# Kernel optimization log

Measured on AMD Instinct MI355X. Metric: run time of the kernel, lower is better.

## Reference

```python
import jax, jax.numpy as jnp
import numpy as np

B, HOR, L, A, HID = 4096, 32, 512, 64, 1024


def _linear_params(key, fan_in, fan_out):
    kw, kb = jax.random.split(key)
    bound = 1.0 / np.sqrt(fan_in)
    W = jax.random.uniform(kw, (fan_in, fan_out), jnp.float32, -bound, bound)
    b = jax.random.uniform(kb, (fan_out,), jnp.float32, -bound, bound)
    return W, b


def setup_inputs() -> dict:
    key = jax.random.key(0)
    ks = jax.random.split(key, 11)
    initial_state = jax.random.normal(ks[0], (B, L), jnp.float32)
    action_sequence = jax.random.normal(ks[1], (B, HOR, A), jnp.float32)
    Wae, bae = _linear_params(ks[2], A, A)
    Wt1, bt1 = _linear_params(ks[3], L + A, HID)
    Wt2, bt2 = _linear_params(ks[4], HID, HID)
    Wt3, bt3 = _linear_params(ks[5], HID, L)
    Wo1, bo1 = _linear_params(ks[6], L, HID)
    Wo2, bo2 = _linear_params(ks[7], HID, L)
    Wh1, bh1 = _linear_params(ks[8], L + A, HID)
    Wh2, bh2 = _linear_params(ks[9], HID, 1)
    return dict(initial_state=initial_state, action_sequence=action_sequence,
                Wae=Wae, bae=bae, Wt1=Wt1, bt1=bt1, Wt2=Wt2, bt2=bt2,
                Wt3=Wt3, bt3=bt3, Wo1=Wo1, bo1=bo1, Wo2=Wo2, bo2=bo2,
                Wh1=Wh1, bh1=bh1, Wh2=Wh2, bh2=bh2)


def reference(initial_state, action_sequence, Wae, bae, Wt1, bt1, Wt2, bt2,
              Wt3, bt3, Wo1, bo1, Wo2, bo2, Wh1, bh1, Wh2, bh2):
    # rollout: sequential scan over horizon steps
    def step(state, action):
        # harm predictor on raw (state, action)
        sa = jnp.concatenate([state, action], axis=-1)            # [B, L+A]
        harm = jax.nn.sigmoid(jax.nn.relu(sa @ Wh1 + bh1) @ Wh2 + bh2)  # [B,1]
        # observation predictor on current state
        obs = jax.nn.relu(state @ Wo1 + bo1) @ Wo2 + bo2          # [B, L]
        # transition on (state, encoded action); residual update
        ae = action @ Wae + bae                                   # [B, A]
        sae = jnp.concatenate([state, ae], axis=-1)               # [B, L+A]
        h = jax.nn.relu(sae @ Wt1 + bt1)
        h = jax.nn.relu(h @ Wt2 + bt2)
        next_state = state + h @ Wt3 + bt3                        # [B, L]
        return next_state, (next_state, obs, harm[:, 0])

    actions_t = jnp.swapaxes(action_sequence, 0, 1)               # [HOR, B, A]
    _, (states_t, obs_t, harm_t) = jax.lax.scan(step, initial_state, actions_t)
    # states: initial + all next states -> [B, HOR+1, L]
    states = jnp.concatenate([initial_state[:, None, :],
                              jnp.swapaxes(states_t, 0, 1)], axis=1)
    observations = jnp.swapaxes(obs_t, 0, 1)                      # [B, HOR, L]
    harm_predictions = jnp.swapaxes(harm_t, 0, 1)                 # [B, HOR]
    return states, observations, harm_predictions
```

## Files before the change

kernel.cpp:

```cpp
#include <hip/hip_runtime.h>
#include <math.h>

#define B_ 4096
#define HOR_ 32
#define L_ 512
#define A_ 64
#define HID_ 1024

#define CB 512
#define MC (CB * HOR_)

typedef unsigned short ushort_t;
typedef __attribute__((ext_vector_type(4))) float f32x4;
typedef __attribute__((ext_vector_type(8))) short s16x8;
typedef __attribute__((ext_vector_type(4))) short s16x4;
typedef __attribute__((ext_vector_type(8))) _Float16 f16x8;

__device__ __forceinline__ unsigned short bf16_rne(float x) {
    unsigned u = __builtin_bit_cast(unsigned, x);
    u += 0x7fffu + ((u >> 16) & 1u);
    return (unsigned short)(u >> 16);
}
__device__ __forceinline__ float bf16_to_f32(unsigned short h) {
    unsigned u = ((unsigned)h) << 16;
    return __builtin_bit_cast(float, u);
}

__device__ __forceinline__ int xcd_swz(int bid, int nwg) {
    return (bid & 7) * (nwg >> 3) + (bid >> 3);
}

__device__ __forceinline__ void gld16(const void* g, void* l) {
    __builtin_amdgcn_global_load_lds(
        (const __attribute__((address_space(1))) void*)g,
        (__attribute__((address_space(3))) void*)l, 16, 0, 0);
}

template <int BMT, bool TWOSRC, bool SPLIT_OUT, bool RELU, bool RESID, bool F32OUT>
__global__ __launch_bounds__(512, 4) void trans_gemm(
    const _Float16* __restrict__ Ahi, const _Float16* __restrict__ Alo,
    int lda, int K,
    const float* __restrict__ Aae, int lda_ae, int aoff,
    const _Float16* __restrict__ Whi, const _Float16* __restrict__ Wlo,
    const float* __restrict__ bias,
    const float* __restrict__ resid, int ldr,
    _Float16* __restrict__ Ohi, _Float16* __restrict__ Olo, int ldoh,
    float* __restrict__ Of, int ldof)
{
    __shared__ _Float16 Ah[2][BMT][32];
    __shared__ _Float16 Al[2][BMT][32];
    __shared__ _Float16 Bh[2][64][32];
    __shared__ _Float16 Bl[2][64][32];

    const int gx = gridDim.x;
    const int bid = xcd_swz(blockIdx.y * gx + blockIdx.x, gx * gridDim.y);
    const int m0 = (bid / gx) * BMT;
    const int n0 = (bid % gx) * 64;

    const int tid = threadIdx.x;
    const int w = tid >> 6, l = tid & 63;
    const int wr = w >> 1, wc = w & 1;
    const int kg = l >> 4, lr = l & 15;
    constexpr int AF = BMT / 64;

    const bool doA = (BMT == 128) || (tid < 256);
    const bool doB = (BMT == 128) ? (tid < 256) : (tid >= 256);
    const int srowA = tid >> 2;
    const int srowB = (BMT == 128) ? (tid >> 2) : ((tid - 256) >> 2);
    const int sg = tid & 3;

    f32x4 acc[AF][2] = {};
    float4 e0, e1;

    const _Float16* pAh = Ahi + (size_t)(m0 + srowA) * lda + sg * 8;
    const _Float16* pAl = Alo + (size_t)(m0 + srowA) * lda + sg * 8;
    const _Float16* pBh = Whi + (size_t)(n0 + srowB) * K + sg * 8;
    const _Float16* pBl = Wlo + (size_t)(n0 + srowB) * K + sg * 8;
    const float* pAe = TWOSRC
        ? (Aae + (size_t)(m0 + srowA) * lda_ae + aoff + sg * 8 - L_)
        : nullptr;

    auto stage = [&](int buf, int ks) {
        const int k0 = ks * 32;
        if (doB) {
            gld16(pBh + k0, &Bh[buf][srowB][sg * 8]);
            gld16(pBl + k0, &Bl[buf][srowB][sg * 8]);
        }
        if (doA && (!TWOSRC || k0 < L_)) {
            gld16(pAh + k0, &Ah[buf][srowA][sg * 8]);
            gld16(pAl + k0, &Al[buf][srowA][sg * 8]);
        }
    };

    const int NT = K / 32;
    stage(0, 0);
    __syncthreads();
    int cur = 0;

    for (int ks = 0; ks < NT; ++ks) {
        const bool havepf = (ks + 1 < NT);
        const int k0n = (ks + 1) * 32;
        const bool aeNext = TWOSRC && havepf && (k0n >= L_);

        if (havepf) {
            stage(cur ^ 1, ks + 1);
            if (aeNext && doA) {
                e0 = *reinterpret_cast<const float4*>(pAe + k0n);
                e1 = *reinterpret_cast<const float4*>(pAe + k0n + 4);
            }
        }

        f16x8 ah[AF], al[AF], bh[2], bl[2];
#pragma unroll
        for (int i = 0; i < AF; ++i) {
            int r = wr * (BMT / 4) + i * 16 + lr;
            ah[i] = *reinterpret_cast<const f16x8*>(&Ah[cur][r][kg * 8]);
            al[i] = *reinterpret_cast<const f16x8*>(&Al[cur][r][kg * 8]);
        }
#pragma unroll
        for (int j = 0; j < 2; ++j) {
            int r = wc * 32 + j * 16 + lr;
            bh[j] = *reinterpret_cast<const f16x8*>(&Bh[cur][r][kg * 8]);
            bl[j] = *reinterpret_cast<const f16x8*>(&Bl[cur][r][kg * 8]);
        }
#pragma unroll
        for (int i = 0; i < AF; ++i)
#pragma unroll
            for (int j = 0; j < 2; ++j) {
                acc[i][j] = __builtin_amdgcn_mfma_f32_16x16x32_f16(
                    ah[i], bh[j], acc[i][j], 0, 0, 0);
                acc[i][j] = __builtin_amdgcn_mfma_f32_16x16x32_f16(
                    ah[i], bl[j], acc[i][j], 0, 0, 0);
                acc[i][j] = __builtin_amdgcn_mfma_f32_16x16x32_f16(
                    al[i], bh[j], acc[i][j], 0, 0, 0);
            }

        if (havepf) {
            if (aeNext && doA) {
                float vv[8] = {e0.x, e0.y, e0.z, e0.w, e1.x, e1.y, e1.z, e1.w};
                f16x8 h, lo;
#pragma unroll
                for (int j = 0; j < 8; ++j) {
                    _Float16 hh = (_Float16)vv[j];
                    h[j] = hh;
                    lo[j] = (_Float16)(vv[j] - (float)hh);
                }
                *reinterpret_cast<f16x8*>(&Ah[cur ^ 1][srowA][sg * 8]) = h;
                *reinterpret_cast<f16x8*>(&Al[cur ^ 1][srowA][sg * 8]) = lo;
            }
            __syncthreads();
            cur ^= 1;
        }
    }

    float bv[2];
#pragma unroll
    for (int j = 0; j < 2; ++j) bv[j] = bias[n0 + wc * 32 + j * 16 + lr];

#pragma unroll
    for (int i = 0; i < AF; ++i)
#pragma unroll
        for (int j = 0; j < 2; ++j)
#pragma unroll
            for (int r = 0; r < 4; ++r) {
                int row = m0 + wr * (BMT / 4) + i * 16 + kg * 4 + r;
                int col = n0 + wc * 32 + j * 16 + lr;
                float v = acc[i][j][r] + bv[j];
                if (RESID)
                    v += resid[(size_t)row * ldr + col];
                if (RELU) v = fmaxf(v, 0.f);
                if (F32OUT)
                    Of[(size_t)row * ldof + col] = v;
                if (SPLIT_OUT) {
                    _Float16 h = (_Float16)v;
                    Ohi[(size_t)row * ldoh + col] = h;
                    Olo[(size_t)row * ldoh + col] = (_Float16)(v - (float)h);
                }
            }
}

__global__ __launch_bounds__(256) void split_transpose(
    const float* __restrict__ W, _Float16* __restrict__ Whi,
    _Float16* __restrict__ Wlo, int K, int N)
{
    int k = blockIdx.x * 256 + threadIdx.x;
    int n = blockIdx.y;
    if (k < K) {
        float v = W[(size_t)k * N + n];
        _Float16 h = (_Float16)v;
        Whi[(size_t)n * K + k] = h;
        Wlo[(size_t)n * K + k] = (_Float16)(v - (float)h);
    }
}

__global__ __launch_bounds__(256) void ae_all(
    const float* __restrict__ actions,
    const float* __restrict__ Wae,
    const float* __restrict__ bae,
    float* __restrict__ ae)
{
    const long r = (long)blockIdx.x * 4 + (threadIdx.x >> 6);
    const int c = threadIdx.x & 63;
    const float* arow = actions + r * 64;
    float acc = bae[c];
#pragma unroll 16
    for (int k = 0; k < 64; ++k) acc = fmaf(arow[k], Wae[k * 64 + c], acc);
    ae[r * 64 + c] = acc;
}

__global__ __launch_bounds__(256) void ae_step(
    const float* __restrict__ actions, const float* __restrict__ Wae,
    const float* __restrict__ bae, int t, float* __restrict__ aeS)
{
    const long b = (long)blockIdx.x * 4 + (threadIdx.x >> 6);
    const int c = threadIdx.x & 63;
    const float* arow = actions + (b * HOR_ + t) * 64;
    float acc = bae[c];
#pragma unroll 16
    for (int k = 0; k < 64; ++k) acc = fmaf(arow[k], Wae[k * 64 + c], acc);
    aeS[b * 64 + c] = acc;
}

__global__ __launch_bounds__(256) void init_split(
    const float* __restrict__ init, float* __restrict__ states,
    _Float16* __restrict__ sth, _Float16* __restrict__ stl)
{
    size_t i = (size_t)blockIdx.x * 256 + threadIdx.x;
    size_t b = i >> 9, l = i & 511;
    float v = init[i];
    states[b * (33 * L_) + l] = v;
    _Float16 h = (_Float16)v;
    sth[i] = h;
    stl[i] = (_Float16)(v - (float)h);
}


__global__ __launch_bounds__(256) void cast_transpose(
    const float* __restrict__ W, ushort_t* __restrict__ WT, int K, int N)
{
    int k = blockIdx.x * 256 + threadIdx.x;
    int n = blockIdx.y;
    if (k < K) WT[(long)n * K + k] = bf16_rne(W[(long)k * N + n]);
}

__global__ __launch_bounds__(256) void mm_split(
    const float* __restrict__ Astate,
    const float* __restrict__ Aact,
    int Ktot,
    const ushort_t* __restrict__ WT,
    int N,
    const float* __restrict__ bias,
    ushort_t* __restrict__ Out)
{
    __shared__ ushort_t Ahi[128][40];
    __shared__ ushort_t Alo[128][40];
    __shared__ ushort_t Bt[128][40];

    const int tid = threadIdx.x;
    const int gx = gridDim.x;
    const int bid = xcd_swz(blockIdx.y * gx + blockIdx.x, gx * gridDim.y);
    const int m0 = (bid / gx) * 128;
    const int n0 = (bid % gx) * 128;
    const int w = tid >> 6;
    const int l = tid & 63;
    const int wm = w >> 1, wn = w & 1;
    const int kg = l >> 4, lr = l & 15;

    f32x4 acc[4][4] = {};

    for (int k0 = 0; k0 < Ktot; k0 += 32) {
#pragma unroll
        for (int s = 0; s < 4; ++s) {
            int idx = tid + s * 256;
            int arow = idx >> 3;
            int ch = idx & 7;
            int m = m0 + arow;
            const float* src;
            if (k0 < L_) {
                src = Astate + (long)((m >> 5) * 33 + (m & 31)) * L_ + k0 + ch * 4;
            } else {
                src = Aact + (long)m * A_ + (k0 - L_) + ch * 4;
            }
            float4 v = *reinterpret_cast<const float4*>(src);
            unsigned short h0 = bf16_rne(v.x), h1 = bf16_rne(v.y),
                           h2 = bf16_rne(v.z), h3 = bf16_rne(v.w);
            unsigned short e0 = bf16_rne(v.x - bf16_to_f32(h0));
            unsigned short e1 = bf16_rne(v.y - bf16_to_f32(h1));
            unsigned short e2 = bf16_rne(v.z - bf16_to_f32(h2));
            unsigned short e3 = bf16_rne(v.w - bf16_to_f32(h3));
            s16x4 hv = {(short)h0, (short)h1, (short)h2, (short)h3};
            s16x4 lv = {(short)e0, (short)e1, (short)e2, (short)e3};
            *reinterpret_cast<s16x4*>(&Ahi[arow][ch * 4]) = hv;
            *reinterpret_cast<s16x4*>(&Alo[arow][ch * 4]) = lv;
        }
#pragma unroll
        for (int s = 0; s < 2; ++s) {
            int idx = tid + s * 256;
            int brow = idx >> 2;
            int ch = idx & 3;
            s16x8 wv = *reinterpret_cast<const s16x8*>(
                &WT[(long)(n0 + brow) * Ktot + k0 + ch * 8]);
            *reinterpret_cast<s16x8*>(&Bt[brow][ch * 8]) = wv;
        }
        __syncthreads();

        s16x8 ah[4], al[4], bb[4];
#pragma unroll
        for (int i = 0; i < 4; ++i) {
            int r = wm * 64 + i * 16 + lr;
            ah[i] = *reinterpret_cast<const s16x8*>(&Ahi[r][kg * 8]);
            al[i] = *reinterpret_cast<const s16x8*>(&Alo[r][kg * 8]);
        }
#pragma unroll
        for (int j = 0; j < 4; ++j) {
            int r = wn * 64 + j * 16 + lr;
            bb[j] = *reinterpret_cast<const s16x8*>(&Bt[r][kg * 8]);
        }
#pragma unroll
        for (int i = 0; i < 4; ++i)
#pragma unroll
            for (int j = 0; j < 4; ++j) {
                acc[i][j] = __builtin_amdgcn_mfma_f32_16x16x32_bf16(
                    ah[i], bb[j], acc[i][j], 0, 0, 0);
                acc[i][j] = __builtin_amdgcn_mfma_f32_16x16x32_bf16(
                    al[i], bb[j], acc[i][j], 0, 0, 0);
            }
        __syncthreads();
    }

    float bv[4];
#pragma unroll
    for (int j = 0; j < 4; ++j) bv[j] = bias[n0 + wn * 64 + j * 16 + lr];
#pragma unroll
    for (int i = 0; i < 4; ++i)
#pragma unroll
        for (int j = 0; j < 4; ++j)
#pragma unroll
            for (int r = 0; r < 4; ++r) {
                int row = m0 + wm * 64 + i * 16 + kg * 4 + r;
                int col = n0 + wn * 64 + j * 16 + lr;
                float v = fmaxf(acc[i][j][r] + bv[j], 0.f);
                Out[(long)row * N + col] = bf16_rne(v);
            }
}

__global__ __launch_bounds__(256) void mm_bf16(
    const ushort_t* __restrict__ Abf,
    const ushort_t* __restrict__ WT,
    int N,
    const float* __restrict__ bias,
    float* __restrict__ Out)
{
    __shared__ ushort_t At[128][40];
    __shared__ ushort_t Bt[128][40];

    const int tid = threadIdx.x;
    const int gx = gridDim.x;
    const int bid = xcd_swz(blockIdx.y * gx + blockIdx.x, gx * gridDim.y);
    const int m0 = (bid / gx) * 128;
    const int n0 = (bid % gx) * 128;
    const int w = tid >> 6;
    const int l = tid & 63;
    const int wm = w >> 1, wn = w & 1;
    const int kg = l >> 4, lr = l & 15;

    f32x4 acc[4][4] = {};

    for (int k0 = 0; k0 < HID_; k0 += 32) {
#pragma unroll
        for (int s = 0; s < 2; ++s) {
            int idx = tid + s * 256;
            int arow = idx >> 2;
            int ch = idx & 3;
            s16x8 av = *reinterpret_cast<const s16x8*>(
                &Abf[(long)(m0 + arow) * HID_ + k0 + ch * 8]);
            *reinterpret_cast<s16x8*>(&At[arow][ch * 8]) = av;
        }
#pragma unroll
        for (int s = 0; s < 2; ++s) {
            int idx = tid + s * 256;
            int brow = idx >> 2;
            int ch = idx & 3;
            s16x8 wv = *reinterpret_cast<const s16x8*>(
                &WT[(long)(n0 + brow) * HID_ + k0 + ch * 8]);
            *reinterpret_cast<s16x8*>(&Bt[brow][ch * 8]) = wv;
        }
        __syncthreads();

        s16x8 aa[4], bb[4];
#pragma unroll
        for (int i = 0; i < 4; ++i)
            aa[i] = *reinterpret_cast<const s16x8*>(&At[wm * 64 + i * 16 + lr][kg * 8]);
#pragma unroll
        for (int j = 0; j < 4; ++j)
            bb[j] = *reinterpret_cast<const s16x8*>(&Bt[wn * 64 + j * 16 + lr][kg * 8]);
#pragma unroll
        for (int i = 0; i < 4; ++i)
#pragma unroll
            for (int j = 0; j < 4; ++j)
                acc[i][j] = __builtin_amdgcn_mfma_f32_16x16x32_bf16(
                    aa[i], bb[j], acc[i][j], 0, 0, 0);
        __syncthreads();
    }

    float bv[4];
#pragma unroll
    for (int j = 0; j < 4; ++j) bv[j] = bias[n0 + wn * 64 + j * 16 + lr];
#pragma unroll
    for (int i = 0; i < 4; ++i)
#pragma unroll
        for (int j = 0; j < 4; ++j)
#pragma unroll
            for (int r = 0; r < 4; ++r) {
                int row = m0 + wm * 64 + i * 16 + kg * 4 + r;
                int col = n0 + wn * 64 + j * 16 + lr;
                Out[(long)row * N + col] = acc[i][j][r] + bv[j];
            }
}

__global__ __launch_bounds__(256) void harm_reduce(
    const ushort_t* __restrict__ hh,
    const float* __restrict__ Wh2,
    const float* __restrict__ bh2,
    float* __restrict__ harm)
{
    const int wave = threadIdx.x >> 6;
    const int lane = threadIdx.x & 63;
    const long r = (long)blockIdx.x * 4 + wave;
    const ushort_t* row = hh + r * HID_;
    float s = 0.f;
#pragma unroll
    for (int q = 0; q < 2; ++q) {
        s16x8 a = *reinterpret_cast<const s16x8*>(&row[lane * 16 + q * 8]);
        float4 w0 = *reinterpret_cast<const float4*>(&Wh2[lane * 16 + q * 8]);
        float4 w1 = *reinterpret_cast<const float4*>(&Wh2[lane * 16 + q * 8 + 4]);
        s = fmaf(bf16_to_f32((unsigned short)a[0]), w0.x, s);
        s = fmaf(bf16_to_f32((unsigned short)a[1]), w0.y, s);
        s = fmaf(bf16_to_f32((unsigned short)a[2]), w0.z, s);
        s = fmaf(bf16_to_f32((unsigned short)a[3]), w0.w, s);
        s = fmaf(bf16_to_f32((unsigned short)a[4]), w1.x, s);
        s = fmaf(bf16_to_f32((unsigned short)a[5]), w1.y, s);
        s = fmaf(bf16_to_f32((unsigned short)a[6]), w1.z, s);
        s = fmaf(bf16_to_f32((unsigned short)a[7]), w1.w, s);
    }
#pragma unroll
    for (int off = 32; off; off >>= 1) s += __shfl_down(s, off);
    if (lane == 0) {
        float x = s + bh2[0];
        harm[r] = 1.f / (1.f + expf(-x));
    }
}

extern "C" void kernel_launch(void* const* d_in, const int* in_sizes, int n_in,
                              void* d_out, int out_size, void* d_ws, size_t ws_size,
                              hipStream_t stream)
{
    const float* initial = (const float*)d_in[0];
    const float* actions = (const float*)d_in[1];
    const float* Wae = (const float*)d_in[2];
    const float* bae = (const float*)d_in[3];
    const float* Wt1 = (const float*)d_in[4];
    const float* bt1 = (const float*)d_in[5];
    const float* Wt2 = (const float*)d_in[6];
    const float* bt2 = (const float*)d_in[7];
    const float* Wt3 = (const float*)d_in[8];
    const float* bt3 = (const float*)d_in[9];
    const float* Wo1 = (const float*)d_in[10];
    const float* bo1 = (const float*)d_in[11];
    const float* Wo2 = (const float*)d_in[12];
    const float* bo2 = (const float*)d_in[13];
    const float* Wh1 = (const float*)d_in[14];
    const float* bh1 = (const float*)d_in[15];
    const float* Wh2 = (const float*)d_in[16];
    const float* bh2 = (const float*)d_in[17];

    float* out = (float*)d_out;
    float* states = out;
    float* obs = out + (size_t)B_ * 33 * L_;
    float* harm = obs + (size_t)B_ * HOR_ * L_;

    char* wsb = (char*)d_ws;
    size_t off = 0;
    auto alloc = [&](size_t bytes) { char* q = wsb + off; off += bytes; return q; };
    ushort_t* WT_o1 = (ushort_t*)alloc((size_t)HID_ * L_ * 2);
    ushort_t* WT_o2 = (ushort_t*)alloc((size_t)L_ * HID_ * 2);
    ushort_t* WT_h1 = (ushort_t*)alloc((size_t)HID_ * 576 * 2);
    _Float16* Wt1h = (_Float16*)alloc((size_t)HID_ * 576 * 2);
    _Float16* Wt1l = (_Float16*)alloc((size_t)HID_ * 576 * 2);
    _Float16* Wt2h = (_Float16*)alloc((size_t)HID_ * HID_ * 2);
    _Float16* Wt2l = (_Float16*)alloc((size_t)HID_ * HID_ * 2);
    _Float16* Wt3h = (_Float16*)alloc((size_t)L_ * HID_ * 2);
    _Float16* Wt3l = (_Float16*)alloc((size_t)L_ * HID_ * 2);
    _Float16* sth  = (_Float16*)alloc((size_t)B_ * L_ * 2);
    _Float16* stl  = (_Float16*)alloc((size_t)B_ * L_ * 2);
    _Float16* h1h  = (_Float16*)alloc((size_t)B_ * HID_ * 2);
    _Float16* h1l  = (_Float16*)alloc((size_t)B_ * HID_ * 2);
    _Float16* h2h  = (_Float16*)alloc((size_t)B_ * HID_ * 2);
    _Float16* h2l  = (_Float16*)alloc((size_t)B_ * HID_ * 2);
    float* ae = (float*)alloc(0);
    const size_t need_batched = off + (size_t)B_ * HOR_ * A_ * 4;
    const bool batched_ae = (ws_size >= need_batched);

    ushort_t* oh = (ushort_t*)h1h;

    cast_transpose<<<dim3(2, HID_), 256, 0, stream>>>(Wo1, WT_o1, L_, HID_);
    cast_transpose<<<dim3(4, L_), 256, 0, stream>>>(Wo2, WT_o2, HID_, L_);
    cast_transpose<<<dim3(3, HID_), 256, 0, stream>>>(Wh1, WT_h1, 576, HID_);
    split_transpose<<<dim3(3, HID_), 256, 0, stream>>>(Wt1, Wt1h, Wt1l, 576, HID_);
    split_transpose<<<dim3(4, HID_), 256, 0, stream>>>(Wt2, Wt2h, Wt2l, HID_, HID_);
    split_transpose<<<dim3(4, L_), 256, 0, stream>>>(Wt3, Wt3h, Wt3l, HID_, L_);

    init_split<<<(B_ * L_) / 256, 256, 0, stream>>>(initial, states, sth, stl);
    if (batched_ae)
        ae_all<<<(B_ * HOR_) / 4, 256, 0, stream>>>(actions, Wae, bae, ae);

    const int ldS = 33 * L_;
    const int lda_ae = batched_ae ? (HOR_ * A_) : A_;

    for (int t = 0; t < HOR_; ++t) {
        if (!batched_ae)
            ae_step<<<B_ / 4, 256, 0, stream>>>(actions, Wae, bae, t, ae);
        const int aoff = batched_ae ? t * A_ : 0;
        trans_gemm<128, true, true, true, false, false>
            <<<dim3(HID_ / 64, B_ / 128), 512, 0, stream>>>(
            sth, stl, L_, 576, ae, lda_ae, aoff,
            Wt1h, Wt1l, bt1, nullptr, 0, h1h, h1l, HID_, nullptr, 0);
        trans_gemm<128, false, true, true, false, false>
            <<<dim3(HID_ / 64, B_ / 128), 512, 0, stream>>>(
            h1h, h1l, HID_, HID_, nullptr, 0, 0,
            Wt2h, Wt2l, bt2, nullptr, 0, h2h, h2l, HID_, nullptr, 0);
        trans_gemm<64, false, true, false, true, true>
            <<<dim3(L_ / 64, B_ / 64), 512, 0, stream>>>(
            h2h, h2l, HID_, HID_, nullptr, 0, 0,
            Wt3h, Wt3l, bt3, states + (size_t)t * L_, ldS,
            sth, stl, L_, states + (size_t)(t + 1) * L_, ldS);
    }

    for (int c = 0; c < B_ / CB; ++c) {
        const float* Sc = states + (size_t)c * CB * 33 * L_;
        const float* Ac = actions + (size_t)c * CB * HOR_ * A_;
        mm_split<<<dim3(HID_ / 128, MC / 128), 256, 0, stream>>>(
            Sc, nullptr, L_, WT_o1, HID_, bo1, oh);
        mm_bf16<<<dim3(L_ / 128, MC / 128), 256, 0, stream>>>(
            oh, WT_o2, L_, bo2, obs + (size_t)c * CB * HOR_ * L_);
        mm_split<<<dim3(HID_ / 128, MC / 128), 256, 0, stream>>>(
            Sc, Ac, 576, WT_h1, HID_, bh1, oh);
        harm_reduce<<<MC / 4, 256, 0, stream>>>(
            oh, Wh2, bh2, harm + (size_t)c * CB * HOR_);
    }
}
```

Before: 3.924 ms.

## Pre-split post-rollout inputs to bf16 hi/lo and use double-buffered async GEMM

Adds a split_chunk pass that converts each chunk's states and actions once into bf16 hi/lo buffers. A new templated mm2 kernel (512 threads, double-buffered LDS with gld16 async loads) then runs the observation and harm GEMMs, so the per-tile float conversion done in mm_split goes away and global loads overlap with MFMA work. Scratch buffers are aliased onto the sth and ae workspace, and the old kernels remain as a fallback when workspace is small. The cost is an extra conversion kernel, extra memory traffic for the hi/lo copies, and a dependence on that buffer aliasing being safe.

Result: faster. 3.704 ms (-5.6%).

```diff
diff --git a/kernel.cpp b/kernel.cpp
--- a/kernel.cpp
+++ b/kernel.cpp
@@ -194,10 +194,8 @@
 }
 
 __global__ __launch_bounds__(256) void ae_all(
-    const float* __restrict__ actions,
-    const float* __restrict__ Wae,
-    const float* __restrict__ bae,
-    float* __restrict__ ae)
+    const float* __restrict__ actions, const float* __restrict__ Wae,
+    const float* __restrict__ bae, float* __restrict__ ae)
 {
     const long r = (long)blockIdx.x * 4 + (threadIdx.x >> 6);
     const int c = threadIdx.x & 63;
@@ -243,24 +241,141 @@
     if (k < K) WT[(long)n * K + k] = bf16_rne(W[(long)k * N + n]);
 }
 
-__global__ __launch_bounds__(256) void mm_split(
-    const float* __restrict__ Astate,
-    const float* __restrict__ Aact,
-    int Ktot,
+__global__ __launch_bounds__(256) void split_chunk(
+    const float* __restrict__ Sc,
+    const float* __restrict__ Ac,
+    ushort_t* __restrict__ Hi,
+    ushort_t* __restrict__ Lo)
+{
+    size_t i = (size_t)blockIdx.x * 256 + threadIdx.x;
+    int m = (int)(i / 144);
+    int g = (int)(i % 144);
+    const float* src = (g < 128)
+        ? Sc + ((size_t)(m >> 5) * 33 + (m & 31)) * L_ + g * 4
+        : Ac + (size_t)m * A_ + (g - 128) * 4;
+    float4 v = *reinterpret_cast<const float4*>(src);
+    unsigned short h0 = bf16_rne(v.x), h1 = bf16_rne(v.y),
+                   h2 = bf16_rne(v.z), h3 = bf16_rne(v.w);
+    unsigned short e0 = bf16_rne(v.x - bf16_to_f32(h0));
+    unsigned short e1 = bf16_rne(v.y - bf16_to_f32(h1));
+    unsigned short e2 = bf16_rne(v.z - bf16_to_f32(h2));
+    unsigned short e3 = bf16_rne(v.w - bf16_to_f32(h3));
+    s16x4 hv = {(short)h0, (short)h1, (short)h2, (short)h3};
+    s16x4 lv = {(short)e0, (short)e1, (short)e2, (short)e3};
+    *reinterpret_cast<s16x4*>(&Hi[(size_t)m * 576 + g * 4]) = hv;
+    *reinterpret_cast<s16x4*>(&Lo[(size_t)m * 576 + g * 4]) = lv;
+}
+
+template <bool SPLITA, bool RELU, bool BF16OUT>
+__global__ __launch_bounds__(512, 4) void mm2(
+    const ushort_t* __restrict__ Ahi_g, const ushort_t* __restrict__ Alo_g,
+    int lda, int K,
     const ushort_t* __restrict__ WT,
-    int N,
     const float* __restrict__ bias,
-    ushort_t* __restrict__ Out)
-{
-    __shared__ ushort_t Ahi[128][40];
-    __shared__ ushort_t Alo[128][40];
-    __shared__ ushort_t Bt[128][40];
-
-    const int tid = threadIdx.x;
+    ushort_t* __restrict__ Ob, float* __restrict__ Of, int N)
+{
+    __shared__ ushort_t Ah[2][128][32];
+    __shared__ ushort_t Al[SPLITA ? 2 : 1][128][32];
+    __shared__ ushort_t Bt[2][128][32];
+
     const int gx = gridDim.x;
     const int bid = xcd_swz(blockIdx.y * gx + blockIdx.x, gx * gridDim.y);
     const int m0 = (bid / gx) * 128;
     const int n0 = (bid % gx) * 128;
+
+    const int tid = threadIdx.x;
+    const int w = tid >> 6, l = tid & 63;
+    const int wr = w >> 1, wc = w & 1;
+    const int kg = l >> 4, lr = l & 15;
+
+    const int srow = tid >> 2, sg = tid & 3;
+
+    f32x4 acc[2][4] = {};
+
+    const ushort_t* pA0 = Ahi_g + (size_t)(m0 + srow) * lda + sg * 8;
+    const ushort_t* pA1 = SPLITA
+        ? (Alo_g + (size_t)(m0 + srow) * lda + sg * 8) : nullptr;
+    const ushort_t* pB = WT + (size_t)(n0 + srow) * K + sg * 8;
+
+    auto stage = [&](int buf, int ks) {
+        const int k0 = ks * 32;
+        gld16(pB + k0, &Bt[buf][srow][sg * 8]);
+        gld16(pA0 + k0, &Ah[buf][srow][sg * 8]);
+        if (SPLITA) gld16(pA1 + k0, &Al[SPLITA ? buf : 0][srow][sg * 8]);
+    };
+
+    const int NT = K / 32;
+    stage(0, 0);
+    __syncthreads();
+    int cur = 0;
+
+    for (int ks = 0; ks < NT; ++ks) {
+        if (ks + 1 < NT) stage(cur ^ 1, ks + 1);
+
+        s16x8 ah[2], al[2], bb[4];
+#pragma unroll
+        for (int i = 0; i < 2; ++i) {
+            int r = wr * 32 + i * 16 + lr;
+            ah[i] = *reinterpret_cast<const s16x8*>(&Ah[cur][r][kg * 8]);
+            if (SPLITA)
+                al[i] = *reinterpret_cast<const s16x8*>(
+                    &Al[SPLITA ? cur : 0][r][kg * 8]);
+        }
+#pragma unroll
+        for (int j = 0; j < 4; ++j) {
+            int r = wc * 64 + j * 16 + lr;
+            bb[j] = *reinterpret_cast<const s16x8*>(&Bt[cur][r][kg * 8]);
+        }
+#pragma unroll
+        for (int i = 0; i < 2; ++i)
+#pragma unroll
+            for (int j = 0; j < 4; ++j) {
+                acc[i][j] = __builtin_amdgcn_mfma_f32_16x16x32_bf16(
+                    ah[i], bb[j], acc[i][j], 0, 0, 0);
+                if (SPLITA)
+                    acc[i][j] = __builtin_amdgcn_mfma_f32_16x16x32_bf16(
+                        al[i], bb[j], acc[i][j], 0, 0, 0);
+            }
+
+        if (ks + 1 < NT) {
+            __syncthreads();
+            cur ^= 1;
+        }
+    }
+
+    float bv[4];
+#pragma unroll
+    for (int j = 0; j < 4; ++j) bv[j] = bias[n0 + wc * 64 + j * 16 + lr];
+
+#pragma unroll
+    for (int i = 0; i < 2; ++i)
+#pragma unroll
+        for (int j = 0; j < 4; ++j)
+#pragma unroll
+            for (int r = 0; r < 4; ++r) {
+                int row = m0 + wr * 32 + i * 16 + kg * 4 + r;
+                int col = n0 + wc * 64 + j * 16 + lr;
+                float v = acc[i][j][r] + bv[j];
+                if (RELU) v = fmaxf(v, 0.f);
+                if (BF16OUT)
+                    Ob[(size_t)row * N + col] = bf16_rne(v);
+                else
+                    Of[(size_t)row * N + col] = v;
+            }
+}
+
+__global__ __launch_bounds__(256) void mm_split(
+    const float* __restrict__ Astate, const float* __restrict__ Aact,
+    int Ktot, const ushort_t* __restrict__ WT, int N,
+    const float* __restrict__ bias, ushort_t* __restrict__ Out)
+{
+    __shared__ ushort_t Ahi[128][40];
+    __shared__ ushort_t Alo[128][40];
+    __shared__ ushort_t Bt[128][40];
+
+    const int tid = threadIdx.x;
+    const int m0 = blockIdx.y * 128;
+    const int n0 = blockIdx.x * 128;
     const int w = tid >> 6;
     const int l = tid & 63;
     const int wm = w >> 1, wn = w & 1;
@@ -345,20 +460,15 @@
 }
 
 __global__ __launch_bounds__(256) void mm_bf16(
-    const ushort_t* __restrict__ Abf,
-    const ushort_t* __restrict__ WT,
-    int N,
-    const float* __restrict__ bias,
-    float* __restrict__ Out)
+    const ushort_t* __restrict__ Abf, const ushort_t* __restrict__ WT,
+    int N, const float* __restrict__ bias, float* __restrict__ Out)
 {
     __shared__ ushort_t At[128][40];
     __shared__ ushort_t Bt[128][40];
 
     const int tid = threadIdx.x;
-    const int gx = gridDim.x;
-    const int bid = xcd_swz(blockIdx.y * gx + blockIdx.x, gx * gridDim.y);
-    const int m0 = (bid / gx) * 128;
-    const int n0 = (bid % gx) * 128;
+    const int m0 = blockIdx.y * 128;
+    const int n0 = blockIdx.x * 128;
     const int w = tid >> 6;
     const int l = tid & 63;
     const int wm = w >> 1, wn = w & 1;
@@ -419,10 +529,8 @@
 }
 
 __global__ __launch_bounds__(256) void harm_reduce(
-    const ushort_t* __restrict__ hh,
-    const float* __restrict__ Wh2,
-    const float* __restrict__ bh2,
-    float* __restrict__ harm)
+    const ushort_t* __restrict__ hh, const float* __restrict__ Wh2,
+    const float* __restrict__ bh2, float* __restrict__ harm)
 {
     const int wave = threadIdx.x >> 6;
     const int lane = threadIdx.x & 63;
@@ -501,7 +609,10 @@
     const size_t need_batched = off + (size_t)B_ * HOR_ * A_ * 4;
     const bool batched_ae = (ws_size >= need_batched);
 
-    ushort_t* oh = (ushort_t*)h1h;
+    ushort_t* Ach_hi = (ushort_t*)sth;
+    ushort_t* Ach_lo = Ach_hi + (size_t)MC * 576;
+    ushort_t* oh2 = (ushort_t*)ae;
+    ushort_t* oh_fb = (ushort_t*)h1h;
 
     cast_transpose<<<dim3(2, HID_), 256, 0, stream>>>(Wo1, WT_o1, L_, HID_);
     cast_transpose<<<dim3(4, L_), 256, 0, stream>>>(Wo2, WT_o2, HID_, L_);
@@ -539,13 +650,27 @@
     for (int c = 0; c < B_ / CB; ++c) {
         const float* Sc = states + (size_t)c * CB * 33 * L_;
         const float* Ac = actions + (size_t)c * CB * HOR_ * A_;
-        mm_split<<<dim3(HID_ / 128, MC / 128), 256, 0, stream>>>(
-            Sc, nullptr, L_, WT_o1, HID_, bo1, oh);
-        mm_bf16<<<dim3(L_ / 128, MC / 128), 256, 0, stream>>>(
-            oh, WT_o2, L_, bo2, obs + (size_t)c * CB * HOR_ * L_);
-        mm_split<<<dim3(HID_ / 128, MC / 128), 256, 0, stream>>>(
-            Sc, Ac, 576, WT_h1, HID_, bh1, oh);
-        harm_reduce<<<MC / 4, 256, 0, stream>>>(
-            oh, Wh2, bh2, harm + (size_t)c * CB * HOR_);
-    }
-}
+        if (batched_ae) {
+            split_chunk<<<(MC * 144) / 256, 256, 0, stream>>>(
+                Sc, Ac, Ach_hi, Ach_lo);
+            mm2<true, true, true><<<dim3(HID_ / 128, MC / 128), 512, 0, stream>>>(
+                Ach_hi, Ach_lo, 576, L_, WT_o1, bo1, oh2, nullptr, HID_);
+            mm2<false, false, false><<<dim3(L_ / 128, MC / 128), 512, 0, stream>>>(
+                oh2, nullptr, HID_, HID_, WT_o2, bo2, nullptr,
+                obs + (size_t)c * CB * HOR_ * L_, L_);
+            mm2<true, true, true><<<dim3(HID_ / 128, MC / 128), 512, 0, stream>>>(
+                Ach_hi, Ach_lo, 576, 576, WT_h1, bh1, oh2, nullptr, HID_);
+            harm_reduce<<<MC / 4, 256, 0, stream>>>(
+                oh2, Wh2, bh2, harm + (size_t)c * CB * HOR_);
+        } else {
+            mm_split<<<dim3(HID_ / 128, MC / 128), 256, 0, stream>>>(
+                Sc, nullptr, L_, WT_o1, HID_, bo1, oh_fb);
+            mm_bf16<<<dim3(L_ / 128, MC / 128), 256, 0, stream>>>(
+                oh_fb, WT_o2, L_, bo2, obs + (size_t)c * CB * HOR_ * L_);
+            mm_split<<<dim3(HID_ / 128, MC / 128), 256, 0, stream>>>(
+                Sc, Ac, 576, WT_h1, HID_, bh1, oh_fb);
+            harm_reduce<<<MC / 4, 256, 0, stream>>>(
+                oh_fb, Wh2, bh2, harm + (size_t)c * CB * HOR_);
+        }
+    }
+}
```
